# Kernel tuning notes

Measured on AMD Instinct MI355X. Metric: run time of the kernel, lower is better.

The kernel has to match this reference:

```python
import jax, jax.numpy as jnp
import numpy as np

N_NODES = 50000
N_EDGES = 800000
D_IN, D_HID, D_OUT = 64, 128, 64


def _graph_conv(x, src, dst, w_rel, w_root, b):
    # PyG GraphConv with aggr='sum':
    #   out_i = W_rel @ sum_{j in N(i)} x_j + W_root @ x_i + b
    # Aggregate first at input width (sum commutes with the linear map),
    # then apply the two linear transforms.
    agg = jax.ops.segment_sum(x[src], dst, num_segments=x.shape[0])  # [N, d_in]
    return agg @ w_rel + x @ w_root + b


def setup_inputs() -> dict:
    key = jax.random.key(0)
    ks = jax.random.split(key, 9)
    x = jax.random.normal(ks[0], (N_NODES, D_IN), dtype=jnp.float32)
    edge_index = jax.random.randint(ks[1], (2, N_EDGES), 0, N_NODES, dtype=jnp.int64)

    def glorot(k, fan_in, fan_out):
        s = jnp.sqrt(2.0 / (fan_in + fan_out)).astype(jnp.float32)
        return jax.random.normal(k, (fan_in, fan_out), dtype=jnp.float32) * s

    return {
        "x": x,
        "edge_index": edge_index,
        "w_rel1": glorot(ks[2], D_IN, D_HID),  "w_root1": glorot(ks[3], D_IN, D_HID),  "b1": jnp.zeros((D_HID,), jnp.float32),
        "w_rel2": glorot(ks[4], D_HID, D_HID), "w_root2": glorot(ks[5], D_HID, D_HID), "b2": jnp.zeros((D_HID,), jnp.float32),
        "w_rel3": glorot(ks[6], D_HID, D_OUT), "w_root3": glorot(ks[7], D_HID, D_OUT), "b3": jnp.zeros((D_OUT,), jnp.float32),
    }


def reference(x, edge_index, w_rel1, w_root1, b1, w_rel2, w_root2, b2, w_rel3, w_root3, b3):
    src, dst = edge_index[0], edge_index[1]
    h = jax.nn.relu(_graph_conv(x, src, dst, w_rel1, w_root1, b1))
    h = jax.nn.relu(_graph_conv(h, src, dst, w_rel2, w_root2, b2))
    out = _graph_conv(h, src, dst, w_rel3, w_root3, b3)  # final layer: no relu
    return out
```

## Files before the change

### kernel.cpp

```cpp
#include <hip/hip_runtime.h>
#include <hip/hip_bf16.h>


#define N_D_IN 64
#define N_D_HID 128
#define N_D_OUT 64

__global__ void detect_kernel(const unsigned int* __restrict__ w, int* __restrict__ flag) {
    __shared__ int nonzero;
    if (threadIdx.x == 0) nonzero = 0;
    __syncthreads();
    for (int i = threadIdx.x; i < 1024; i += 256) {
        if (w[2 * i + 1] != 0u) atomicOr(&nonzero, 1);
    }
    __syncthreads();
    if (threadIdx.x == 0) *flag = (nonzero ? 0 : 1);
}

__device__ __forceinline__ int load_edge(const void* edge, const int* flag, size_t idx) {
    if (*flag) return (int)((const long long*)edge)[idx];
    return ((const int*)edge)[idx];
}

__global__ void hist_kernel(const void* __restrict__ edge, const int* __restrict__ flag,
                            int* __restrict__ cnt, int n_edges) {
    int i = blockIdx.x * 256 + threadIdx.x;
    if (i >= n_edges) return;
    int d = load_edge(edge, flag, (size_t)n_edges + i);
    atomicAdd(&cnt[d], 1);
}

__global__ __launch_bounds__(256) void blocksum_kernel(const int* __restrict__ cnt,
                                                       int* __restrict__ bsum, int n) {
    int i = blockIdx.x * 256 + threadIdx.x;
    int v = (i < n) ? cnt[i] : 0;
#pragma unroll
    for (int off = 1; off < 64; off <<= 1) v += __shfl_xor(v, off);
    __shared__ int wsums[4];
    if ((threadIdx.x & 63) == 0) wsums[threadIdx.x >> 6] = v;
    __syncthreads();
    if (threadIdx.x == 0) bsum[blockIdx.x] = wsums[0] + wsums[1] + wsums[2] + wsums[3];
}

__global__ __launch_bounds__(1024) void scan_bsum_kernel(const int* __restrict__ bsum,
                                                         int* __restrict__ boff, int nb) {
    __shared__ int tmp[1024];
    int t = threadIdx.x;
    int v = (t < nb) ? bsum[t] : 0;
    tmp[t] = v;
    __syncthreads();
    for (int off = 1; off < 1024; off <<= 1) {
        int u = (t >= off) ? tmp[t - off] : 0;
        __syncthreads();
        tmp[t] += u;
        __syncthreads();
    }
    if (t < nb) boff[t] = tmp[t] - v;
}

__global__ __launch_bounds__(256) void emit_kernel(const int* __restrict__ cnt,
                                                   const int* __restrict__ boff,
                                                   int* __restrict__ row_ptr,
                                                   int* __restrict__ cursor, int n) {
    __shared__ int tmp[256];
    int b = blockIdx.x, t = threadIdx.x;
    int i = b * 256 + t;
    int v = (i < n) ? cnt[i] : 0;
    tmp[t] = v;
    __syncthreads();
    for (int off = 1; off < 256; off <<= 1) {
        int u = (t >= off) ? tmp[t - off] : 0;
        __syncthreads();
        tmp[t] += u;
        __syncthreads();
    }
    int excl = tmp[t] - v + boff[b];
    if (i < n) {
        row_ptr[i] = excl;
        cursor[i] = excl;
        if (i == n - 1) row_ptr[n] = excl + v;
    }
}

__global__ void scatter_kernel(const void* __restrict__ edge, const int* __restrict__ flag,
                               int* __restrict__ cursor, int* __restrict__ srcs, int n_edges) {
    int i = blockIdx.x * 256 + threadIdx.x;
    if (i >= n_edges) return;
    int s = load_edge(edge, flag, (size_t)i);
    int d = load_edge(edge, flag, (size_t)n_edges + i);
    int pos = atomicAdd(&cursor[d], 1);
    srcs[pos] = s;
}

template <int D, bool ADD_BASE>
__global__ __launch_bounds__(256) void agg_kernel(const float* __restrict__ in,
                                                  const float* __restrict__ base,
                                                  float* __restrict__ out,
                                                  const int* __restrict__ row_ptr,
                                                  const int* __restrict__ srcs, int n_nodes) {
    constexpr int LPR = D / 4;
    constexpr int SLOTS = 64 / LPR;
    const int node = blockIdx.x * 4 + (threadIdx.x >> 6);
    if (node >= n_nodes) return;
    const int lane = threadIdx.x & 63;
    const int c4 = lane % LPR;
    const int slot = lane / LPR;
    const int e0 = row_ptr[node], e1 = row_ptr[node + 1];
    float4 acc = make_float4(0.f, 0.f, 0.f, 0.f);
    for (int e = e0 + slot; e < e1; e += SLOTS) {
        int s = srcs[e];
        float4 v = *(const float4*)&in[(size_t)s * D + c4 * 4];
        acc.x += v.x; acc.y += v.y; acc.z += v.z; acc.w += v.w;
    }
#pragma unroll
    for (int off = LPR; off < 64; off <<= 1) {
        acc.x += __shfl_xor(acc.x, off);
        acc.y += __shfl_xor(acc.y, off);
        acc.z += __shfl_xor(acc.z, off);
        acc.w += __shfl_xor(acc.w, off);
    }
    if (lane < LPR) {
        if (ADD_BASE) {
            float4 b = *(const float4*)&base[(size_t)node * D + c4 * 4];
            acc.x += b.x; acc.y += b.y; acc.z += b.z; acc.w += b.w;
        }
        *(float4*)&out[(size_t)node * D + c4 * 4] = acc;
    }
}

template <int DIN, int DOUT, int TM, bool DUAL, bool RELU, bool BIAS>
__global__ __launch_bounds__(256) void gemm_kernel(const float* __restrict__ A,
                                                   const float* __restrict__ B,
                                                   const float* __restrict__ W1,
                                                   const float* __restrict__ W2,
                                                   const float* __restrict__ bias,
                                                   float* __restrict__ out, int n_nodes) {
    constexpr int JS = DOUT / 4;
    constexpr int NL = 256 / JS;
    constexpr int BN = NL * TM;
    constexpr int K4 = DIN / 4;

    const int tid = threadIdx.x;
    const int j0 = (tid % JS) * 4;
    const int n0 = blockIdx.x * BN + (tid / JS) * TM;

    size_t arow[TM];
#pragma unroll
    for (int m = 0; m < TM; ++m) {
        int n = n0 + m;
        if (n > n_nodes - 1) n = n_nodes - 1;
        arow[m] = (size_t)n * DIN * 4;
    }

    float acc[TM][4];
#pragma unroll
    for (int m = 0; m < TM; ++m)
#pragma unroll
        for (int c = 0; c < 4; ++c) acc[m][c] = 0.f;

#pragma unroll 4
    for (int k4 = 0; k4 < K4; ++k4) {
        float w1s[4][4], w2s[4][4];
#pragma unroll
        for (int u = 0; u < 4; ++u) {
            float4 t = *(const float4*)&W1[(size_t)(k4 * 4 + u) * DOUT + j0];
            w1s[u][0] = t.x; w1s[u][1] = t.y; w1s[u][2] = t.z; w1s[u][3] = t.w;
            if constexpr (DUAL) {
                float4 t2 = *(const float4*)&W2[(size_t)(k4 * 4 + u) * DOUT + j0];
                w2s[u][0] = t2.x; w2s[u][1] = t2.y; w2s[u][2] = t2.z; w2s[u][3] = t2.w;
            }
        }
#pragma unroll
        for (int m = 0; m < TM; ++m) {
            float4 a4 = *(const float4*)((const char*)A + arow[m] + (size_t)k4 * 16);
            float av[4] = {a4.x, a4.y, a4.z, a4.w};
#pragma unroll
            for (int c = 0; c < 4; ++c)
#pragma unroll
                for (int u = 0; u < 4; ++u) acc[m][c] += av[u] * w1s[u][c];
            if constexpr (DUAL) {
                float4 b4 = *(const float4*)((const char*)B + arow[m] + (size_t)k4 * 16);
                float bv4[4] = {b4.x, b4.y, b4.z, b4.w};
#pragma unroll
                for (int c = 0; c < 4; ++c)
#pragma unroll
                    for (int u = 0; u < 4; ++u) acc[m][c] += bv4[u] * w2s[u][c];
            }
        }
    }

    float bv[4] = {0.f, 0.f, 0.f, 0.f};
    if constexpr (BIAS) {
        float4 t = *(const float4*)&bias[j0];
        bv[0] = t.x; bv[1] = t.y; bv[2] = t.z; bv[3] = t.w;
    }
#pragma unroll
    for (int m = 0; m < TM; ++m) {
        int gn = n0 + m;
        if (gn < n_nodes) {
            float v0 = acc[m][0] + bv[0], v1 = acc[m][1] + bv[1];
            float v2 = acc[m][2] + bv[2], v3 = acc[m][3] + bv[3];
            if constexpr (RELU) {
                v0 = fmaxf(v0, 0.f); v1 = fmaxf(v1, 0.f);
                v2 = fmaxf(v2, 0.f); v3 = fmaxf(v3, 0.f);
            }
            float4 o; o.x = v0; o.y = v1; o.z = v2; o.w = v3;
            *(float4*)&out[(size_t)gn * DOUT + j0] = o;
        }
    }
}

template <int DIN, int DOUT, int TM>
__global__ __launch_bounds__(256) void gemm2out_kernel(const float* __restrict__ A,
                                                       const float* __restrict__ W1,
                                                       const float* __restrict__ W2,
                                                       const float* __restrict__ bias,
                                                       float* __restrict__ o1,
                                                       float* __restrict__ o2, int n_nodes) {
    constexpr int JS = DOUT / 4;
    constexpr int NL = 256 / JS;
    constexpr int BN = NL * TM;
    constexpr int K4 = DIN / 4;

    const int tid = threadIdx.x;
    const int j0 = (tid % JS) * 4;
    const int n0 = blockIdx.x * BN + (tid / JS) * TM;

    size_t arow[TM];
#pragma unroll
    for (int m = 0; m < TM; ++m) {
        int n = n0 + m;
        if (n > n_nodes - 1) n = n_nodes - 1;
        arow[m] = (size_t)n * DIN * 4;
    }

    float acc1[TM][4], acc2[TM][4];
#pragma unroll
    for (int m = 0; m < TM; ++m)
#pragma unroll
        for (int c = 0; c < 4; ++c) { acc1[m][c] = 0.f; acc2[m][c] = 0.f; }

#pragma unroll 4
    for (int k4 = 0; k4 < K4; ++k4) {
        float w1s[4][4], w2s[4][4];
#pragma unroll
        for (int u = 0; u < 4; ++u) {
            float4 t = *(const float4*)&W1[(size_t)(k4 * 4 + u) * DOUT + j0];
            w1s[u][0] = t.x; w1s[u][1] = t.y; w1s[u][2] = t.z; w1s[u][3] = t.w;
            float4 t2 = *(const float4*)&W2[(size_t)(k4 * 4 + u) * DOUT + j0];
            w2s[u][0] = t2.x; w2s[u][1] = t2.y; w2s[u][2] = t2.z; w2s[u][3] = t2.w;
        }
#pragma unroll
        for (int m = 0; m < TM; ++m) {
            float4 a4 = *(const float4*)((const char*)A + arow[m] + (size_t)k4 * 16);
            float av[4] = {a4.x, a4.y, a4.z, a4.w};
#pragma unroll
            for (int c = 0; c < 4; ++c)
#pragma unroll
                for (int u = 0; u < 4; ++u) {
                    acc1[m][c] += av[u] * w1s[u][c];
                    acc2[m][c] += av[u] * w2s[u][c];
                }
        }
    }

    float4 bt = *(const float4*)&bias[j0];
    float bv[4] = {bt.x, bt.y, bt.z, bt.w};
#pragma unroll
    for (int m = 0; m < TM; ++m) {
        int gn = n0 + m;
        if (gn < n_nodes) {
            float4 q;
            q.x = acc1[m][0]; q.y = acc1[m][1]; q.z = acc1[m][2]; q.w = acc1[m][3];
            *(float4*)&o1[(size_t)gn * DOUT + j0] = q;
            float4 r;
            r.x = acc2[m][0] + bv[0]; r.y = acc2[m][1] + bv[1];
            r.z = acc2[m][2] + bv[2]; r.w = acc2[m][3] + bv[3];
            *(float4*)&o2[(size_t)gn * DOUT + j0] = r;
        }
    }
}

extern "C" void kernel_launch(void* const* d_in, const int* in_sizes, int n_in,
                              void* d_out, int out_size, void* d_ws, size_t ws_size,
                              hipStream_t stream) {
    const float* x = (const float*)d_in[0];
    const void* edge = d_in[1];
    const float* w_rel1 = (const float*)d_in[2];
    const float* w_root1 = (const float*)d_in[3];
    const float* b1 = (const float*)d_in[4];
    const float* w_rel2 = (const float*)d_in[5];
    const float* w_root2 = (const float*)d_in[6];
    const float* b2 = (const float*)d_in[7];
    const float* w_rel3 = (const float*)d_in[8];
    const float* w_root3 = (const float*)d_in[9];
    const float* b3 = (const float*)d_in[10];
    float* out = (float*)d_out;

    const int n_nodes = in_sizes[0] / N_D_IN;
    const int n_edges = in_sizes[1] / 2;

    char* ws = (char*)d_ws;
    int* cnt = (int*)(ws + 0);
    int* row_ptr = (int*)(ws + (1 << 20));
    int* cursor = (int*)(ws + (2 << 20));
    int* flag = (int*)(ws + (3 << 20));
    int* bsum = (int*)(ws + (3 << 20) + 1024);
    int* boff = (int*)(ws + (3 << 20) + 1024 + 4096);
    int* srcs = (int*)(ws + (4 << 20));
    float* agg = (float*)(ws + (size_t)(8 << 20));
    float* h1 = (float*)(ws + (size_t)(34 << 20));
    float* h2 = (float*)(ws + (size_t)(60 << 20));
    float* t3 = (float*)(ws + (size_t)(34 << 20));
    float* base3 = (float*)(ws + (size_t)(47 << 20));

    const int eblk = (n_edges + 255) / 256;
    const int nblk = (n_nodes + 255) / 256;
    const int ablk = (n_nodes + 3) / 4;

    hipMemsetAsync(cnt, 0, (size_t)n_nodes * sizeof(int), stream);
    detect_kernel<<<1, 256, 0, stream>>>((const unsigned int*)edge, flag);
    hist_kernel<<<eblk, 256, 0, stream>>>(edge, flag, cnt, n_edges);
    blocksum_kernel<<<nblk, 256, 0, stream>>>(cnt, bsum, n_nodes);
    scan_bsum_kernel<<<1, 1024, 0, stream>>>(bsum, boff, nblk);
    emit_kernel<<<nblk, 256, 0, stream>>>(cnt, boff, row_ptr, cursor, n_nodes);
    scatter_kernel<<<eblk, 256, 0, stream>>>(edge, flag, cursor, srcs, n_edges);

    const int g128 = (n_nodes + 63) / 64;
    const int g64 = (n_nodes + 63) / 64;

    agg_kernel<64, false><<<ablk, 256, 0, stream>>>(x, nullptr, agg, row_ptr, srcs, n_nodes);
    gemm_kernel<64, 128, 8, true, true, true><<<g128, 256, 0, stream>>>(
        agg, x, w_rel1, w_root1, b1, h1, n_nodes);

    agg_kernel<128, false><<<ablk, 256, 0, stream>>>(h1, nullptr, agg, row_ptr, srcs, n_nodes);
    gemm_kernel<128, 128, 8, true, true, true><<<g128, 256, 0, stream>>>(
        agg, h1, w_rel2, w_root2, b2, h2, n_nodes);

    gemm2out_kernel<128, 64, 4><<<g64, 256, 0, stream>>>(
        h2, w_rel3, w_root3, b3, t3, base3, n_nodes);
    agg_kernel<64, true><<<ablk, 256, 0, stream>>>(t3, base3, out, row_ptr, srcs, n_nodes);
}
```

Measured before the change: 529.4 us.

## Stage GEMM input rows and weight tiles in shared memory with K-tiling

Replaces the two register-only GEMM kernels with one templated kernel. Each 256-thread block of 32 nodes cooperatively loads 32-wide K slices of the activations and both weight matrices into LDS, then computes from LDS. This is meant to turn scattered per-thread global loads of weights and rows into coalesced loads with reuse across the block. In exchange it adds two barriers per K tile, smaller node tiles (more blocks, more weight reloads per node), and LDS bank-conflict risk on the row-wise sA reads.

Result: faster. 450.4 us (-14.9%).

```diff
diff --git a/kernel.cpp b/kernel.cpp
--- a/kernel.cpp
+++ b/kernel.cpp
@@ -128,155 +128,130 @@
     }
 }
 
-template <int DIN, int DOUT, int TM, bool DUAL, bool RELU, bool BIAS>
-__global__ __launch_bounds__(256) void gemm_kernel(const float* __restrict__ A,
-                                                   const float* __restrict__ B,
-                                                   const float* __restrict__ W1,
-                                                   const float* __restrict__ W2,
-                                                   const float* __restrict__ bias,
-                                                   float* __restrict__ out, int n_nodes) {
+template <int DIN, int DOUT, int MODE, bool RELU>
+__global__ __launch_bounds__(256) void gemm_tiled(const float* __restrict__ A,
+                                                  const float* __restrict__ B,
+                                                  const float* __restrict__ W1,
+                                                  const float* __restrict__ W2,
+                                                  const float* __restrict__ bias,
+                                                  float* __restrict__ o1,
+                                                  float* __restrict__ o2, int n_nodes) {
+    constexpr int BN = 32;
+    constexpr int KT = 32;
     constexpr int JS = DOUT / 4;
     constexpr int NL = 256 / JS;
-    constexpr int BN = NL * TM;
-    constexpr int K4 = DIN / 4;
+    constexpr int TM = BN / NL;
+    constexpr int NKT = DIN / KT;
+    constexpr int K4T = KT / 4;
+    constexpr int W4 = (KT * DOUT / 4) / 256;
+
+    __shared__ float sA[BN][KT];
+    __shared__ float sB[(MODE == 1) ? BN : 1][(MODE == 1) ? KT : 4];
+    __shared__ float sW1[KT][DOUT];
+    __shared__ float sW2[KT][DOUT];
 
     const int tid = threadIdx.x;
-    const int j0 = (tid % JS) * 4;
-    const int n0 = blockIdx.x * BN + (tid / JS) * TM;
-
-    size_t arow[TM];
-#pragma unroll
-    for (int m = 0; m < TM; ++m) {
-        int n = n0 + m;
-        if (n > n_nodes - 1) n = n_nodes - 1;
-        arow[m] = (size_t)n * DIN * 4;
-    }
-
-    float acc[TM][4];
+    const int node0 = blockIdx.x * BN;
+    const int jslot = tid % JS;
+    const int j0 = jslot * 4;
+    const int nlane = tid / JS;
+
+    float acc1[TM][4];
+    float acc2[(MODE == 2) ? TM : 1][4];
 #pragma unroll
     for (int m = 0; m < TM; ++m)
 #pragma unroll
-        for (int c = 0; c < 4; ++c) acc[m][c] = 0.f;
-
-#pragma unroll 4
-    for (int k4 = 0; k4 < K4; ++k4) {
-        float w1s[4][4], w2s[4][4];
-#pragma unroll
-        for (int u = 0; u < 4; ++u) {
-            float4 t = *(const float4*)&W1[(size_t)(k4 * 4 + u) * DOUT + j0];
-            w1s[u][0] = t.x; w1s[u][1] = t.y; w1s[u][2] = t.z; w1s[u][3] = t.w;
-            if constexpr (DUAL) {
-                float4 t2 = *(const float4*)&W2[(size_t)(k4 * 4 + u) * DOUT + j0];
+        for (int c = 0; c < 4; ++c) {
+            acc1[m][c] = 0.f;
+            if constexpr (MODE == 2) acc2[m][c] = 0.f;
+        }
+
+    for (int kt = 0; kt < NKT; ++kt) {
+        {
+            int n = tid / K4T, c4 = tid % K4T;
+            int gn = node0 + n;
+            float4 av = make_float4(0.f, 0.f, 0.f, 0.f);
+            float4 bv = make_float4(0.f, 0.f, 0.f, 0.f);
+            if (gn < n_nodes) {
+                av = *(const float4*)&A[(size_t)gn * DIN + kt * KT + c4 * 4];
+                if constexpr (MODE == 1)
+                    bv = *(const float4*)&B[(size_t)gn * DIN + kt * KT + c4 * 4];
+            }
+            *(float4*)&sA[n][c4 * 4] = av;
+            if constexpr (MODE == 1) *(float4*)&sB[n][c4 * 4] = bv;
+        }
+#pragma unroll
+        for (int w = 0; w < W4; ++w) {
+            int idx = w * 256 + tid;
+            int r = idx / (DOUT / 4), c4 = idx % (DOUT / 4);
+            *(float4*)&sW1[r][c4 * 4] =
+                *(const float4*)&W1[(size_t)(kt * KT + r) * DOUT + c4 * 4];
+            *(float4*)&sW2[r][c4 * 4] =
+                *(const float4*)&W2[(size_t)(kt * KT + r) * DOUT + c4 * 4];
+        }
+        __syncthreads();
+
+#pragma unroll
+        for (int k4 = 0; k4 < K4T; ++k4) {
+            float w1s[4][4], w2s[4][4];
+#pragma unroll
+            for (int u = 0; u < 4; ++u) {
+                float4 t = *(const float4*)&sW1[k4 * 4 + u][j0];
+                w1s[u][0] = t.x; w1s[u][1] = t.y; w1s[u][2] = t.z; w1s[u][3] = t.w;
+                float4 t2 = *(const float4*)&sW2[k4 * 4 + u][j0];
                 w2s[u][0] = t2.x; w2s[u][1] = t2.y; w2s[u][2] = t2.z; w2s[u][3] = t2.w;
             }
-        }
-#pragma unroll
-        for (int m = 0; m < TM; ++m) {
-            float4 a4 = *(const float4*)((const char*)A + arow[m] + (size_t)k4 * 16);
-            float av[4] = {a4.x, a4.y, a4.z, a4.w};
-#pragma unroll
-            for (int c = 0; c < 4; ++c)
-#pragma unroll
-                for (int u = 0; u < 4; ++u) acc[m][c] += av[u] * w1s[u][c];
-            if constexpr (DUAL) {
-                float4 b4 = *(const float4*)((const char*)B + arow[m] + (size_t)k4 * 16);
-                float bv4[4] = {b4.x, b4.y, b4.z, b4.w};
-#pragma unroll
-                for (int c = 0; c < 4; ++c)
-#pragma unroll
-                    for (int u = 0; u < 4; ++u) acc[m][c] += bv4[u] * w2s[u][c];
+#pragma unroll
+            for (int m = 0; m < TM; ++m) {
+                int n = nlane * TM + m;
+                float4 a4 = *(const float4*)&sA[n][k4 * 4];
+                float av[4] = {a4.x, a4.y, a4.z, a4.w};
+                if constexpr (MODE == 1) {
+                    float4 b4 = *(const float4*)&sB[n][k4 * 4];
+                    float bv4[4] = {b4.x, b4.y, b4.z, b4.w};
+#pragma unroll
+                    for (int c = 0; c < 4; ++c)
+#pragma unroll
+                        for (int u = 0; u < 4; ++u)
+                            acc1[m][c] += av[u] * w1s[u][c] + bv4[u] * w2s[u][c];
+                } else {
+#pragma unroll
+                    for (int c = 0; c < 4; ++c)
+#pragma unroll
+                        for (int u = 0; u < 4; ++u) {
+                            acc1[m][c] += av[u] * w1s[u][c];
+                            acc2[m][c] += av[u] * w2s[u][c];
+                        }
+                }
             }
         }
-    }
-
-    float bv[4] = {0.f, 0.f, 0.f, 0.f};
-    if constexpr (BIAS) {
-        float4 t = *(const float4*)&bias[j0];
-        bv[0] = t.x; bv[1] = t.y; bv[2] = t.z; bv[3] = t.w;
-    }
-#pragma unroll
-    for (int m = 0; m < TM; ++m) {
-        int gn = n0 + m;
-        if (gn < n_nodes) {
-            float v0 = acc[m][0] + bv[0], v1 = acc[m][1] + bv[1];
-            float v2 = acc[m][2] + bv[2], v3 = acc[m][3] + bv[3];
-            if constexpr (RELU) {
-                v0 = fmaxf(v0, 0.f); v1 = fmaxf(v1, 0.f);
-                v2 = fmaxf(v2, 0.f); v3 = fmaxf(v3, 0.f);
-            }
-            float4 o; o.x = v0; o.y = v1; o.z = v2; o.w = v3;
-            *(float4*)&out[(size_t)gn * DOUT + j0] = o;
-        }
-    }
-}
-
-template <int DIN, int DOUT, int TM>
-__global__ __launch_bounds__(256) void gemm2out_kernel(const float* __restrict__ A,
-                                                       const float* __restrict__ W1,
-                                                       const float* __restrict__ W2,
-                                                       const float* __restrict__ bias,
-                                                       float* __restrict__ o1,
-                                                       float* __restrict__ o2, int n_nodes) {
-    constexpr int JS = DOUT / 4;
-    constexpr int NL = 256 / JS;
-    constexpr int BN = NL * TM;
-    constexpr int K4 = DIN / 4;
-
-    const int tid = threadIdx.x;
-    const int j0 = (tid % JS) * 4;
-    const int n0 = blockIdx.x * BN + (tid / JS) * TM;
-
-    size_t arow[TM];
-#pragma unroll
-    for (int m = 0; m < TM; ++m) {
-        int n = n0 + m;
-        if (n > n_nodes - 1) n = n_nodes - 1;
-        arow[m] = (size_t)n * DIN * 4;
-    }
-
-    float acc1[TM][4], acc2[TM][4];
-#pragma unroll
-    for (int m = 0; m < TM; ++m)
-#pragma unroll
-        for (int c = 0; c < 4; ++c) { acc1[m][c] = 0.f; acc2[m][c] = 0.f; }
-
-#pragma unroll 4
-    for (int k4 = 0; k4 < K4; ++k4) {
-        float w1s[4][4], w2s[4][4];
-#pragma unroll
-        for (int u = 0; u < 4; ++u) {
-            float4 t = *(const float4*)&W1[(size_t)(k4 * 4 + u) * DOUT + j0];
-            w1s[u][0] = t.x; w1s[u][1] = t.y; w1s[u][2] = t.z; w1s[u][3] = t.w;
-            float4 t2 = *(const float4*)&W2[(size_t)(k4 * 4 + u) * DOUT + j0];
-            w2s[u][0] = t2.x; w2s[u][1] = t2.y; w2s[u][2] = t2.z; w2s[u][3] = t2.w;
-        }
-#pragma unroll
-        for (int m = 0; m < TM; ++m) {
-            float4 a4 = *(const float4*)((const char*)A + arow[m] + (size_t)k4 * 16);
-            float av[4] = {a4.x, a4.y, a4.z, a4.w};
-#pragma unroll
-            for (int c = 0; c < 4; ++c)
-#pragma unroll
-                for (int u = 0; u < 4; ++u) {
-                    acc1[m][c] += av[u] * w1s[u][c];
-                    acc2[m][c] += av[u] * w2s[u][c];
-                }
-        }
+        __syncthreads();
     }
 
     float4 bt = *(const float4*)&bias[j0];
     float bv[4] = {bt.x, bt.y, bt.z, bt.w};
 #pragma unroll
     for (int m = 0; m < TM; ++m) {
-        int gn = n0 + m;
+        int gn = node0 + nlane * TM + m;
         if (gn < n_nodes) {
-            float4 q;
-            q.x = acc1[m][0]; q.y = acc1[m][1]; q.z = acc1[m][2]; q.w = acc1[m][3];
-            *(float4*)&o1[(size_t)gn * DOUT + j0] = q;
-            float4 r;
-            r.x = acc2[m][0] + bv[0]; r.y = acc2[m][1] + bv[1];
-            r.z = acc2[m][2] + bv[2]; r.w = acc2[m][3] + bv[3];
-            *(float4*)&o2[(size_t)gn * DOUT + j0] = r;
+            if constexpr (MODE == 1) {
+                float v0 = acc1[m][0] + bv[0], v1 = acc1[m][1] + bv[1];
+                float v2 = acc1[m][2] + bv[2], v3 = acc1[m][3] + bv[3];
+                if constexpr (RELU) {
+                    v0 = fmaxf(v0, 0.f); v1 = fmaxf(v1, 0.f);
+                    v2 = fmaxf(v2, 0.f); v3 = fmaxf(v3, 0.f);
+                }
+                float4 o; o.x = v0; o.y = v1; o.z = v2; o.w = v3;
+                *(float4*)&o1[(size_t)gn * DOUT + j0] = o;
+            } else {
+                float4 q;
+                q.x = acc1[m][0]; q.y = acc1[m][1]; q.z = acc1[m][2]; q.w = acc1[m][3];
+                *(float4*)&o1[(size_t)gn * DOUT + j0] = q;
+                float4 r;
+                r.x = acc2[m][0] + bv[0]; r.y = acc2[m][1] + bv[1];
+                r.z = acc2[m][2] + bv[2]; r.w = acc2[m][3] + bv[3];
+                *(float4*)&o2[(size_t)gn * DOUT + j0] = r;
+            }
         }
     }
 }
@@ -317,6 +292,7 @@
     const int eblk = (n_edges + 255) / 256;
     const int nblk = (n_nodes + 255) / 256;
     const int ablk = (n_nodes + 3) / 4;
+    const int gblk = (n_nodes + 31) / 32;
 
     hipMemsetAsync(cnt, 0, (size_t)n_nodes * sizeof(int), stream);
     detect_kernel<<<1, 256, 0, stream>>>((const unsigned int*)edge, flag);
@@ -326,18 +302,15 @@
     emit_kernel<<<nblk, 256, 0, stream>>>(cnt, boff, row_ptr, cursor, n_nodes);
     scatter_kernel<<<eblk, 256, 0, stream>>>(edge, flag, cursor, srcs, n_edges);
 
-    const int g128 = (n_nodes + 63) / 64;
-    const int g64 = (n_nodes + 63) / 64;
-
     agg_kernel<64, false><<<ablk, 256, 0, stream>>>(x, nullptr, agg, row_ptr, srcs, n_nodes);
-    gemm_kernel<64, 128, 8, true, true, true><<<g128, 256, 0, stream>>>(
-        agg, x, w_rel1, w_root1, b1, h1, n_nodes);
+    gemm_tiled<64, 128, 1, true><<<gblk, 256, 0, stream>>>(
+        agg, x, w_rel1, w_root1, b1, h1, nullptr, n_nodes);
 
     agg_kernel<128, false><<<ablk, 256, 0, stream>>>(h1, nullptr, agg, row_ptr, srcs, n_nodes);
-    gemm_kernel<128, 128, 8, true, true, true><<<g128, 256, 0, stream>>>(
-        agg, h1, w_rel2, w_root2, b2, h2, n_nodes);
-
-    gemm2out_kernel<128, 64, 4><<<g64, 256, 0, stream>>>(
-        h2, w_rel3, w_root3, b3, t3, base3, n_nodes);
+    gemm_tiled<128, 128, 1, true><<<gblk, 256, 0, stream>>>(
+        agg, h1, w_rel2, w_root2, b2, h2, nullptr, n_nodes);
+
+    gemm_tiled<128, 64, 2, false><<<gblk, 256, 0, stream>>>(
+        h2, nullptr, w_rel3, w_root3, b3, t3, base3, n_nodes);
     agg_kernel<64, true><<<ablk, 256, 0, stream>>>(t3, base3, out, row_ptr, srcs, n_nodes);
 }
```
